# Kernel tuning notes

Hardware: AMD Instinct MI355X
Metric: run time of the kernel (lower is better)

## Reference

```python
import jax, jax.numpy as jnp
import numpy as np

PRE_NMS = 2000          # _pre_nms_top_n['testing']
POST_NMS = 1000         # _post_nms_top_n['testing']
NMS_THRESH = 0.7
MIN_SIZE = 1.0
BBOX_XFORM_CLIP = float(np.log(1000.0 / 16.0))  # standard dw/dh clamp


def setup_inputs() -> dict:
    key = jax.random.key(0)
    k1, k2, k3, k4, k5 = jax.random.split(key, 5)
    N = 2_000_000
    H, W = 800, 1333
    # realistic anchors: centers uniform over the image, sizes in [16, 256]
    cx = jax.random.uniform(k1, (N,)) * W
    cy = jax.random.uniform(k2, (N,)) * H
    wh = 16.0 + jax.random.uniform(k3, (N, 2)) * 240.0
    anchor = jnp.stack([cx - wh[:, 0] / 2, cy - wh[:, 1] / 2,
                        cx + wh[:, 0] / 2, cy + wh[:, 1] / 2], axis=1)
    objectness = jax.random.normal(k4, (N,))
    pred_bbox_delta = jax.random.normal(k5, (N, 4)) * 0.1
    return {"anchor": anchor, "objectness": objectness,
            "pred_bbox_delta": pred_bbox_delta, "image_h": H, "image_w": W}


def _decode(delta, anchor):
    # BoxCoder.decode with reg_weights = (1,1,1,1)
    w = anchor[:, 2] - anchor[:, 0]
    h = anchor[:, 3] - anchor[:, 1]
    cx = anchor[:, 0] + 0.5 * w
    cy = anchor[:, 1] + 0.5 * h
    dx, dy, dw, dh = delta[:, 0], delta[:, 1], delta[:, 2], delta[:, 3]
    dw = jnp.minimum(dw, BBOX_XFORM_CLIP)
    dh = jnp.minimum(dh, BBOX_XFORM_CLIP)
    pcx = dx * w + cx
    pcy = dy * h + cy
    pw = jnp.exp(dw) * w
    ph = jnp.exp(dh) * h
    return jnp.stack([pcx - 0.5 * pw, pcy - 0.5 * ph,
                      pcx + 0.5 * pw, pcy + 0.5 * ph], axis=1)


def _greedy_nms_keep(boxes, keep_init):
    # boxes: [K,4] already sorted by descending score; keep_init masks invalid boxes
    K = boxes.shape[0]
    areas = (boxes[:, 2] - boxes[:, 0]) * (boxes[:, 3] - boxes[:, 1])
    idx = jnp.arange(K)

    def body(i, keep):
        b = boxes[i]
        xx1 = jnp.maximum(b[0], boxes[:, 0])
        yy1 = jnp.maximum(b[1], boxes[:, 1])
        xx2 = jnp.minimum(b[2], boxes[:, 2])
        yy2 = jnp.minimum(b[3], boxes[:, 3])
        inter = jnp.maximum(xx2 - xx1, 0.0) * jnp.maximum(yy2 - yy1, 0.0)
        iou = inter / (areas[i] + areas - inter + 1e-9)
        suppress = (iou > NMS_THRESH) & (idx > i) & keep[i]
        return keep & ~suppress

    return jax.lax.fori_loop(0, K, body, keep_init)


def reference(anchor, objectness, pred_bbox_delta, image_h, image_w):
    # 1) top-k pre-NMS selection over all N anchors (memory-bound)
    score, top_idx = jax.lax.top_k(objectness, PRE_NMS)
    a = anchor[top_idx]
    d = pred_bbox_delta[top_idx]
    # 2) box decode
    boxes = _decode(d, a)
    # 3) clip to image (process_box)
    x1 = jnp.clip(boxes[:, 0], 0.0, float(image_w))
    y1 = jnp.clip(boxes[:, 1], 0.0, float(image_h))
    x2 = jnp.clip(boxes[:, 2], 0.0, float(image_w))
    y2 = jnp.clip(boxes[:, 3], 0.0, float(image_h))
    boxes = jnp.stack([x1, y1, x2, y2], axis=1)
    # 4) min-size filter -> mask (fixed shapes under jit)
    valid = ((x2 - x1) >= MIN_SIZE) & ((y2 - y1) >= MIN_SIZE)
    # 5) greedy NMS (boxes are already score-sorted; invalid never kept/suppressing)
    keep = _greedy_nms_keep(boxes, valid)
    # 6) take first POST_NMS kept boxes; pad the rest with zeros
    neg_inf = jnp.float32(-jnp.inf)
    final_score = jnp.where(keep, score, neg_inf)
    fs, fi = jax.lax.top_k(final_score, POST_NMS)
    mask = jnp.isfinite(fs)[:, None].astype(boxes.dtype)
    proposal = boxes[fi] * mask  # [POST_NMS, 4], zero-padded
    return proposal
```

## Files before the change

kernel.cpp:

```cpp
#include <hip/hip_runtime.h>
#include <hip/hip_bf16.h>


typedef unsigned int uint;
typedef unsigned long long ull;

#define PRE_NMS   2000
#define POST_NMS  1000
#define SORT_N    4096
#define NBINS     2048
#define NMS_TH    0.7f
#define MIN_SIZE  1.0f
#define BBOX_CLIP 4.135166556742356f

#define HIST_OFF    0
#define META_OFF    8192
#define VALID_OFF   8448
#define CAND_OFF    8704
#define TOPIDX_OFF  41472
#define BOXES_OFF   49472
#define MASK_OFF    81472
#define REM_OFF     605760
#define ZERO_WORDS  2176

__device__ __forceinline__ uint map_f32(float f) {
    uint u = __float_as_uint(f);
    return u ^ ((u & 0x80000000u) ? 0xFFFFFFFFu : 0x80000000u);
}

__global__ __launch_bounds__(256) void init_kernel(uint* __restrict__ wsHead,
                                                   float4* __restrict__ out) {
    int t = blockIdx.x * 256 + threadIdx.x;
    if (t < ZERO_WORDS) wsHead[t] = 0u;
    if (t < POST_NMS) out[t] = make_float4(0.f, 0.f, 0.f, 0.f);
}

__global__ __launch_bounds__(256) void hist_kernel(const float* __restrict__ obj,
                                                   int n, uint* __restrict__ hist) {
    __shared__ uint h[NBINS];
    for (int b = threadIdx.x; b < NBINS; b += 256) h[b] = 0;
    __syncthreads();
    int n4 = n >> 2;
    const float4* obj4 = reinterpret_cast<const float4*>(obj);
    int stride = gridDim.x * blockDim.x;
    for (int i = blockIdx.x * blockDim.x + threadIdx.x; i < n4; i += stride) {
        float4 v = obj4[i];
        atomicAdd(&h[map_f32(v.x) >> 21], 1u);
        atomicAdd(&h[map_f32(v.y) >> 21], 1u);
        atomicAdd(&h[map_f32(v.z) >> 21], 1u);
        atomicAdd(&h[map_f32(v.w) >> 21], 1u);
    }
    int base = n4 << 2;
    for (int i = base + blockIdx.x * blockDim.x + threadIdx.x; i < n; i += stride)
        atomicAdd(&h[map_f32(obj[i]) >> 21], 1u);
    __syncthreads();
    for (int b = threadIdx.x; b < NBINS; b += 256)
        if (h[b]) atomicAdd(&hist[b], h[b]);
}

__global__ __launch_bounds__(256) void thresh_kernel(const uint* __restrict__ hist,
                                                     uint* __restrict__ meta) {
    __shared__ uint s_sum[256];
    __shared__ uint s_suf[256];
    int t = threadIdx.x;
    uint local[8];
    uint sum = 0;
#pragma unroll 8
    for (int b = 0; b < 8; b++) { local[b] = hist[t * 8 + b]; sum += local[b]; }
    s_sum[t] = sum;
    __syncthreads();
    if (t == 0) {
        uint acc = 0;
        for (int c = 255; c >= 0; c--) { s_suf[c] = acc; acc += s_sum[c]; }
    }
    __syncthreads();
    uint c = s_suf[t];
#pragma unroll 8
    for (int b = 7; b >= 0; b--) {
        uint nc = c + local[b];
        if (c < (uint)PRE_NMS && nc >= (uint)PRE_NMS) meta[0] = (uint)(t * 8 + b);
        c = nc;
    }
}

__global__ __launch_bounds__(256) void collect_kernel(const float* __restrict__ obj,
                                                      int n, uint* __restrict__ meta,
                                                      ull* __restrict__ cand) {
    uint T = meta[0];
    int n4 = n >> 2;
    const float4* obj4 = reinterpret_cast<const float4*>(obj);
    int stride = gridDim.x * blockDim.x;
    for (int i = blockIdx.x * blockDim.x + threadIdx.x; i < n4; i += stride) {
        float4 v = obj4[i];
        uint u0 = map_f32(v.x), u1 = map_f32(v.y), u2 = map_f32(v.z), u3 = map_f32(v.w);
        if ((u0 >> 21) >= T) {
            uint pos = atomicAdd(&meta[1], 1u);
            if (pos < (uint)SORT_N) cand[pos] = ((ull)u0 << 32) | (ull)(~(uint)(i * 4 + 0));
        }
        if ((u1 >> 21) >= T) {
            uint pos = atomicAdd(&meta[1], 1u);
            if (pos < (uint)SORT_N) cand[pos] = ((ull)u1 << 32) | (ull)(~(uint)(i * 4 + 1));
        }
        if ((u2 >> 21) >= T) {
            uint pos = atomicAdd(&meta[1], 1u);
            if (pos < (uint)SORT_N) cand[pos] = ((ull)u2 << 32) | (ull)(~(uint)(i * 4 + 2));
        }
        if ((u3 >> 21) >= T) {
            uint pos = atomicAdd(&meta[1], 1u);
            if (pos < (uint)SORT_N) cand[pos] = ((ull)u3 << 32) | (ull)(~(uint)(i * 4 + 3));
        }
    }
    int base = n4 << 2;
    for (int i = base + blockIdx.x * blockDim.x + threadIdx.x; i < n; i += stride) {
        uint u = map_f32(obj[i]);
        if ((u >> 21) >= T) {
            uint pos = atomicAdd(&meta[1], 1u);
            if (pos < (uint)SORT_N) cand[pos] = ((ull)u << 32) | (ull)(~(uint)i);
        }
    }
}

__global__ __launch_bounds__(1024) void sort_kernel(const ull* __restrict__ cand,
                                                    const uint* __restrict__ meta,
                                                    int* __restrict__ topIdx) {
    __shared__ ull keys[SORT_N];
    uint n = meta[1]; if (n > (uint)SORT_N) n = SORT_N;
    for (int t = threadIdx.x; t < SORT_N; t += 1024)
        keys[t] = (t < (int)n) ? cand[t] : 0ULL;
    __syncthreads();
    for (int k = 2; k <= SORT_N; k <<= 1) {
        for (int j = k >> 1; j > 0; j >>= 1) {
            for (int t = threadIdx.x; t < SORT_N; t += 1024) {
                int ixj = t ^ j;
                if (ixj > t) {
                    ull A = keys[t], B = keys[ixj];
                    bool desc = ((t & k) == 0);
                    if (desc ? (A < B) : (A > B)) { keys[t] = B; keys[ixj] = A; }
                }
            }
            __syncthreads();
        }
    }
    for (int t = threadIdx.x; t < PRE_NMS; t += 1024)
        topIdx[t] = (int)(~(uint)keys[t]);
}

__global__ __launch_bounds__(256) void decode_kernel(const float* __restrict__ anchor,
                                                     const float* __restrict__ delta,
                                                     const int* __restrict__ topIdx,
                                                     const int* __restrict__ imh,
                                                     const int* __restrict__ imw,
                                                     float4* __restrict__ boxes,
                                                     ull* __restrict__ validWords) {
    int i = blockIdx.x * blockDim.x + threadIdx.x;
    if (i >= PRE_NMS) return;
    int idx = topIdx[i];
    const float4 a = reinterpret_cast<const float4*>(anchor)[idx];
    const float4 d = reinterpret_cast<const float4*>(delta)[idx];
    float W = (float)imw[0], H = (float)imh[0];
    float w  = a.z - a.x;
    float h  = a.w - a.y;
    float cx = a.x + 0.5f * w;
    float cy = a.y + 0.5f * h;
    float dw = fminf(d.z, BBOX_CLIP);
    float dh = fminf(d.w, BBOX_CLIP);
    float pcx = d.x * w + cx;
    float pcy = d.y * h + cy;
    float pw  = expf(dw) * w;
    float ph  = expf(dh) * h;
    float x1 = fminf(fmaxf(pcx - 0.5f * pw, 0.0f), W);
    float y1 = fminf(fmaxf(pcy - 0.5f * ph, 0.0f), H);
    float x2 = fminf(fmaxf(pcx + 0.5f * pw, 0.0f), W);
    float y2 = fminf(fmaxf(pcy + 0.5f * ph, 0.0f), H);
    boxes[i] = make_float4(x1, y1, x2, y2);
    bool valid = (x2 - x1 >= MIN_SIZE) && (y2 - y1 >= MIN_SIZE);
    if (valid) atomicOr(&validWords[i >> 6], 1ULL << (i & 63));
}

__global__ __launch_bounds__(256) void mask_kernel(const float4* __restrict__ boxes,
                                                   ull* __restrict__ gmask) {
    __shared__ float4 b[PRE_NMS];
    for (int t = threadIdx.x; t < PRE_NMS; t += 256) b[t] = boxes[t];
    __syncthreads();
    int tid = blockIdx.x * 256 + threadIdx.x;
    int r = tid >> 5;
    int c = tid & 31;
    ull m = 0;
    if (r < PRE_NMS) {
        float4 bi = b[r];
        float areai = (bi.z - bi.x) * (bi.w - bi.y);
        int j0 = c * 64;
#pragma unroll
        for (int jj = 0; jj < 64; jj++) {
            int j = j0 + jj;
            if (j < PRE_NMS && j > r) {
                float4 bj = b[j];
                float xx1 = fmaxf(bi.x, bj.x), yy1 = fmaxf(bi.y, bj.y);
                float xx2 = fminf(bi.z, bj.z), yy2 = fminf(bi.w, bj.w);
                float inter = fmaxf(xx2 - xx1, 0.0f) * fmaxf(yy2 - yy1, 0.0f);
                float areaj = (bj.z - bj.x) * (bj.w - bj.y);
                float iou = inter / (areai + areaj - inter + 1e-9f);
                if (iou > NMS_TH) m |= (1ULL << jj);
            }
        }
    }
    gmask[tid] = m;
}

__device__ __forceinline__ void nms_stage_tile(const char* gm, void* dst,
                                               int w, int lane) {
    const char* src = gm + (size_t)w * 16384 + (size_t)(lane * 16);
#pragma unroll
    for (int k = 0; k < 16; ++k) {
        __builtin_amdgcn_global_load_lds(
            (const __attribute__((address_space(1))) uint*)(src + k * 1024),
            (__attribute__((address_space(3))) uint*)((char*)dst + k * 1024),
            16, 0, 0);
    }
}

__global__ __launch_bounds__(64) void nms_kernel(const ull* __restrict__ gmask,
                                                 const ull* __restrict__ validWords,
                                                 ull* __restrict__ remOut) {
    __shared__ __align__(16) ull buf[2][2048];
    const int lane = threadIdx.x;
    const int lw = lane & 31;
    const bool hiHalf = lane >= 32;
    ull rem = hiHalf ? 0ULL : ~validWords[lw];
    const char* gm = (const char*)gmask;

    nms_stage_tile(gm, &buf[0][0], 0, lane);

    for (int w = 0; w < 32; ++w) {
        const int b = w & 1;
        if (w + 1 < 32) {
            nms_stage_tile(gm, &buf[b ^ 1][0], w + 1, lane);
            asm volatile("s_waitcnt vmcnt(16)" ::: "memory");
        } else {
            asm volatile("s_waitcnt vmcnt(0)" ::: "memory");
        }
        __builtin_amdgcn_sched_barrier(0);

        const int w32 = w + 32;
        uint r0 = (uint)__builtin_amdgcn_readlane((int)(uint)rem, w);
        uint r1 = (uint)__builtin_amdgcn_readlane((int)(uint)(rem >> 32), w);
        uint r2 = (uint)__builtin_amdgcn_readlane((int)(uint)rem, w32);
        uint r3 = (uint)__builtin_amdgcn_readlane((int)(uint)(rem >> 32), w32);
        ull rw = (((ull)(r1 | r3)) << 32) | (ull)(r0 | r2);

        const char* base = (const char*)&buf[b][0] + (hiHalf ? 256 : 0) + lw * 8;

#pragma unroll
        for (int ch = 0; ch < 4; ++ch) {
            ull o[8];
#pragma unroll
            for (int p = 0; p < 8; ++p)
                o[p] = *(const ull*)(base + (ch * 16 + 2 * p) * 256);
#pragma unroll
            for (int p = 0; p < 8; ++p) {
                const int i0 = ch * 16 + 2 * p, i1 = i0 + 1;
                uint dlo0 = (uint)__builtin_amdgcn_readlane((int)(uint)o[p], w);
                uint dhi0 = (uint)__builtin_amdgcn_readlane((int)(uint)(o[p] >> 32), w);
                uint dlo1 = (uint)__builtin_amdgcn_readlane((int)(uint)o[p], w32);
                uint dhi1 = (uint)__builtin_amdgcn_readlane((int)(uint)(o[p] >> 32), w32);
                ull d0 = (((ull)dhi0) << 32) | dlo0;
                ull d1 = (((ull)dhi1) << 32) | dlo1;
                bool a0 = ((rw >> i0) & 1ULL) == 0ULL;
                rw |= a0 ? d0 : 0ULL;
                bool a1 = ((rw >> i1) & 1ULL) == 0ULL;
                rw |= a1 ? d1 : 0ULL;
                uint m0 = a0 ? ~0u : 0u;
                uint m1 = a1 ? ~0u : 0u;
                uint ms = hiHalf ? m1 : m0;
                rem |= o[p] & ((((ull)ms) << 32) | (ull)ms);
            }
        }
    }
    ull other = __shfl(rem, lane + 32, 64);
    rem |= other;
    if (lane < 32) remOut[lw] = rem;
}

__global__ __launch_bounds__(256) void output_kernel(const float4* __restrict__ boxes,
                                                     const ull* __restrict__ rem,
                                                     float4* __restrict__ out) {
    __shared__ uint pre[33];
    __shared__ ull kept_s[32];
    int t = threadIdx.x;
    if (t < 32) kept_s[t] = ~rem[t];
    __syncthreads();
    if (t == 0) {
        uint acc = 0;
        for (int w = 0; w < 32; w++) { pre[w] = acc; acc += (uint)__popcll(kept_s[w]); }
        pre[32] = acc;
    }
    __syncthreads();
    for (int i = t; i < PRE_NMS; i += 256) {
        ull kw = kept_s[i >> 6];
        if ((kw >> (i & 63)) & 1ULL) {
            uint rank = pre[i >> 6] +
                        (uint)__popcll(kw & ((1ULL << (i & 63)) - 1ULL));
            if (rank < (uint)POST_NMS) out[rank] = boxes[i];
        }
    }
}

extern "C" void kernel_launch(void* const* d_in, const int* in_sizes, int n_in,
                              void* d_out, int out_size, void* d_ws, size_t ws_size,
                              hipStream_t stream) {
    const float* anchor = (const float*)d_in[0];
    const float* obj    = (const float*)d_in[1];
    const float* delta  = (const float*)d_in[2];
    const int*   imh    = (const int*)d_in[3];
    const int*   imw    = (const int*)d_in[4];
    int n = in_sizes[1];

    char* ws = (char*)d_ws;
    uint* hist       = (uint*)(ws + HIST_OFF);
    uint* meta       = (uint*)(ws + META_OFF);
    ull*  validWords = (ull*)(ws + VALID_OFF);
    ull*  cand       = (ull*)(ws + CAND_OFF);
    int*  topIdx     = (int*)(ws + TOPIDX_OFF);
    float4* boxes    = (float4*)(ws + BOXES_OFF);
    ull*  gmask      = (ull*)(ws + MASK_OFF);
    ull*  rem        = (ull*)(ws + REM_OFF);

    init_kernel<<<(ZERO_WORDS + 255) / 256, 256, 0, stream>>>(
        (uint*)ws, (float4*)d_out);
    hist_kernel<<<512, 256, 0, stream>>>(obj, n, hist);
    thresh_kernel<<<1, 256, 0, stream>>>(hist, meta);
    collect_kernel<<<512, 256, 0, stream>>>(obj, n, meta, cand);
    sort_kernel<<<1, 1024, 0, stream>>>(cand, meta, topIdx);
    decode_kernel<<<(PRE_NMS + 255) / 256, 256, 0, stream>>>(
        anchor, delta, topIdx, imh, imw, boxes, validWords);
    mask_kernel<<<(32 * 2048) / 256, 256, 0, stream>>>(boxes, gmask);
    nms_kernel<<<1, 64, 0, stream>>>(gmask, validWords, rem);
    output_kernel<<<1, 256, 0, stream>>>(boxes, rem, (float4*)d_out);
}
```

Baseline: 310.2 us.

## Use compact diagonal mask for NMS serial scan and fuse output into NMS kernel

The mask kernel now also writes the diagonal 64x64 IoU block of each row into a compact array. The NMS kernel resolves intra-block suppression from that array with uniform scalar loads, replacing the per-row readlane chains. It then applies suppression to the remaining rows with a simple branch-free OR loop. The output compaction and zero-padding move into the NMS kernel, which removes the separate output launch and the output zeroing in init. This shortens the serial dependency chain per word and saves one kernel launch. In exchange, the scan relies on scalar global loads of the diag data inside the critical loop.

```diff
diff --git a/kernel.cpp b/kernel.cpp
--- a/kernel.cpp
+++ b/kernel.cpp
@@ -20,7 +20,7 @@
 #define TOPIDX_OFF  41472
 #define BOXES_OFF   49472
 #define MASK_OFF    81472
-#define REM_OFF     605760
+#define DIAG_OFF    605760
 #define ZERO_WORDS  2176
 
 __device__ __forceinline__ uint map_f32(float f) {
@@ -28,11 +28,9 @@
     return u ^ ((u & 0x80000000u) ? 0xFFFFFFFFu : 0x80000000u);
 }
 
-__global__ __launch_bounds__(256) void init_kernel(uint* __restrict__ wsHead,
-                                                   float4* __restrict__ out) {
+__global__ __launch_bounds__(256) void init_kernel(uint* __restrict__ wsHead) {
     int t = blockIdx.x * 256 + threadIdx.x;
     if (t < ZERO_WORDS) wsHead[t] = 0u;
-    if (t < POST_NMS) out[t] = make_float4(0.f, 0.f, 0.f, 0.f);
 }
 
 __global__ __launch_bounds__(256) void hist_kernel(const float* __restrict__ obj,
@@ -178,7 +176,8 @@
 }
 
 __global__ __launch_bounds__(256) void mask_kernel(const float4* __restrict__ boxes,
-                                                   ull* __restrict__ gmask) {
+                                                   ull* __restrict__ gmask,
+                                                   ull* __restrict__ diag) {
     __shared__ float4 b[PRE_NMS];
     for (int t = threadIdx.x; t < PRE_NMS; t += 256) b[t] = boxes[t];
     __syncthreads();
@@ -205,6 +204,7 @@
         }
     }
     gmask[tid] = m;
+    if (c == (r >> 6)) diag[r] = m;
 }
 
 __device__ __forceinline__ void nms_stage_tile(const char* gm, void* dst,
@@ -220,9 +220,13 @@
 }
 
 __global__ __launch_bounds__(64) void nms_kernel(const ull* __restrict__ gmask,
+                                                 const ull* __restrict__ diag,
                                                  const ull* __restrict__ validWords,
-                                                 ull* __restrict__ remOut) {
+                                                 const float4* __restrict__ boxes,
+                                                 float4* __restrict__ out) {
     __shared__ __align__(16) ull buf[2][2048];
+    __shared__ ull kept_s[32];
+    __shared__ uint pre_s[33];
     const int lane = threadIdx.x;
     const int lw = lane & 31;
     const bool hiHalf = lane >= 32;
@@ -248,61 +252,53 @@
         uint r3 = (uint)__builtin_amdgcn_readlane((int)(uint)(rem >> 32), w32);
         ull rw = (((ull)(r1 | r3)) << 32) | (ull)(r0 | r2);
 
+        const ull* dg = diag + w * 64;
+#pragma unroll
+        for (int ch = 0; ch < 4; ++ch) {
+            ull dd[16];
+#pragma unroll
+            for (int q = 0; q < 16; ++q) dd[q] = dg[ch * 16 + q];
+#pragma unroll
+            for (int q = 0; q < 16; ++q) {
+                const int i = ch * 16 + q;
+                rw |= ((rw >> i) & 1ULL) ? 0ULL : dd[q];
+            }
+        }
+
         const char* base = (const char*)&buf[b][0] + (hiHalf ? 256 : 0) + lw * 8;
-
-#pragma unroll
-        for (int ch = 0; ch < 4; ++ch) {
-            ull o[8];
-#pragma unroll
-            for (int p = 0; p < 8; ++p)
-                o[p] = *(const ull*)(base + (ch * 16 + 2 * p) * 256);
-#pragma unroll
-            for (int p = 0; p < 8; ++p) {
-                const int i0 = ch * 16 + 2 * p, i1 = i0 + 1;
-                uint dlo0 = (uint)__builtin_amdgcn_readlane((int)(uint)o[p], w);
-                uint dhi0 = (uint)__builtin_amdgcn_readlane((int)(uint)(o[p] >> 32), w);
-                uint dlo1 = (uint)__builtin_amdgcn_readlane((int)(uint)o[p], w32);
-                uint dhi1 = (uint)__builtin_amdgcn_readlane((int)(uint)(o[p] >> 32), w32);
-                ull d0 = (((ull)dhi0) << 32) | dlo0;
-                ull d1 = (((ull)dhi1) << 32) | dlo1;
-                bool a0 = ((rw >> i0) & 1ULL) == 0ULL;
-                rw |= a0 ? d0 : 0ULL;
-                bool a1 = ((rw >> i1) & 1ULL) == 0ULL;
-                rw |= a1 ? d1 : 0ULL;
-                uint m0 = a0 ? ~0u : 0u;
-                uint m1 = a1 ? ~0u : 0u;
-                uint ms = hiHalf ? m1 : m0;
-                rem |= o[p] & ((((ull)ms) << 32) | (ull)ms);
-            }
+#pragma unroll
+        for (int p = 0; p < 32; ++p) {
+            ull o = *(const ull*)(base + (2 * p) * 256);
+            uint b0 = (uint)(rw >> (2 * p)) & 1u;
+            uint b1 = (uint)(rw >> (2 * p + 1)) & 1u;
+            uint m0 = b0 - 1u;
+            uint m1 = b1 - 1u;
+            uint ms = hiHalf ? m1 : m0;
+            rem |= o & ((((ull)ms) << 32) | (ull)ms);
         }
     }
     ull other = __shfl(rem, lane + 32, 64);
     rem |= other;
-    if (lane < 32) remOut[lw] = rem;
-}
-
-__global__ __launch_bounds__(256) void output_kernel(const float4* __restrict__ boxes,
-                                                     const ull* __restrict__ rem,
-                                                     float4* __restrict__ out) {
-    __shared__ uint pre[33];
-    __shared__ ull kept_s[32];
-    int t = threadIdx.x;
-    if (t < 32) kept_s[t] = ~rem[t];
-    __syncthreads();
-    if (t == 0) {
+
+    if (lane < 32) kept_s[lane] = ~rem;
+    __syncthreads();
+    if (lane == 0) {
         uint acc = 0;
-        for (int w = 0; w < 32; w++) { pre[w] = acc; acc += (uint)__popcll(kept_s[w]); }
-        pre[32] = acc;
-    }
-    __syncthreads();
-    for (int i = t; i < PRE_NMS; i += 256) {
+        for (int t = 0; t < 32; t++) { pre_s[t] = acc; acc += (uint)__popcll(kept_s[t]); }
+        pre_s[32] = acc;
+    }
+    __syncthreads();
+    for (int i = lane; i < PRE_NMS; i += 64) {
         ull kw = kept_s[i >> 6];
         if ((kw >> (i & 63)) & 1ULL) {
-            uint rank = pre[i >> 6] +
+            uint rank = pre_s[i >> 6] +
                         (uint)__popcll(kw & ((1ULL << (i & 63)) - 1ULL));
             if (rank < (uint)POST_NMS) out[rank] = boxes[i];
         }
     }
+    uint keptTotal = pre_s[32];
+    for (uint r = keptTotal + (uint)lane; r < (uint)POST_NMS; r += 64)
+        out[r] = make_float4(0.f, 0.f, 0.f, 0.f);
 }
 
 extern "C" void kernel_launch(void* const* d_in, const int* in_sizes, int n_in,
@@ -323,17 +319,16 @@
     int*  topIdx     = (int*)(ws + TOPIDX_OFF);
     float4* boxes    = (float4*)(ws + BOXES_OFF);
     ull*  gmask      = (ull*)(ws + MASK_OFF);
-    ull*  rem        = (ull*)(ws + REM_OFF);
-
-    init_kernel<<<(ZERO_WORDS + 255) / 256, 256, 0, stream>>>(
-        (uint*)ws, (float4*)d_out);
+    ull*  diag       = (ull*)(ws + DIAG_OFF);
+
+    init_kernel<<<(ZERO_WORDS + 255) / 256, 256, 0, stream>>>((uint*)ws);
     hist_kernel<<<512, 256, 0, stream>>>(obj, n, hist);
     thresh_kernel<<<1, 256, 0, stream>>>(hist, meta);
     collect_kernel<<<512, 256, 0, stream>>>(obj, n, meta, cand);
     sort_kernel<<<1, 1024, 0, stream>>>(cand, meta, topIdx);
     decode_kernel<<<(PRE_NMS + 255) / 256, 256, 0, stream>>>(
         anchor, delta, topIdx, imh, imw, boxes, validWords);
-    mask_kernel<<<(32 * 2048) / 256, 256, 0, stream>>>(boxes, gmask);
-    nms_kernel<<<1, 64, 0, stream>>>(gmask, validWords, rem);
-    output_kernel<<<1, 256, 0, stream>>>(boxes, rem, (float4*)d_out);
-}
+    mask_kernel<<<(32 * 2048) / 256, 256, 0, stream>>>(boxes, gmask, diag);
+    nms_kernel<<<1, 64, 0, stream>>>(gmask, diag, validWords, boxes,
+                                     (float4*)d_out);
+}
```

Measured after the change: 312.0 us. About the same (+0.6%).
